# Kernel tuning notes

Measured on AMD Instinct MI355X. Metric: run time of the kernel, lower is better.

Reference implementation:

```python
import jax, jax.numpy as jnp
import numpy as np

C, H = 256, 256  # feat_num, feat_h (equirect is H x 2H)


def setup_inputs() -> dict:
    key = jax.random.key(0)
    ks = jax.random.split(key, 6)
    m = jax.random.normal(ks[0], (1, C, H, 2 * H), jnp.float32)
    b = jax.random.normal(ks[1], (1, C, H, H), jnp.float32)
    u = jax.random.normal(ks[2], (1, C, H, H), jnp.float32)
    d = jax.random.normal(ks[3], (1, C, H, H), jnp.float32)
    Wf = jax.random.normal(ks[4], (C, C, 3, 3), jnp.float32) * 0.02
    bf = jnp.zeros((C,), jnp.float32)
    Wm = jax.random.normal(ks[5], (1, 2 * C, 1, 1), jnp.float32) * 0.02
    bm = jnp.zeros((1,), jnp.float32)
    return {"m": m, "b": b, "u": u, "d": d, "Wf": Wf, "bf": bf, "Wm": Wm, "bm": bm}


def _cube2equi(cube, out_h, out_w):
    # cube: [6, C, h, h]; face order: 0 back(z-), 1 down(y-), 2 front(z+), 3 left(x-), 4 right(x+), 5 up(y+)
    h = cube.shape[-1]
    theta = (jnp.arange(out_w, dtype=cube.dtype) + 0.5) / out_w * (2.0 * jnp.pi) - jnp.pi  # longitude [-pi, pi)
    phi = jnp.pi / 2 - (jnp.arange(out_h, dtype=cube.dtype) + 0.5) / out_h * jnp.pi        # latitude [pi/2, -pi/2]
    st, ct = jnp.sin(theta)[None, :], jnp.cos(theta)[None, :]
    sp, cp = jnp.sin(phi)[:, None], jnp.cos(phi)[:, None]
    dx = cp * st
    dy = jnp.broadcast_to(sp, (out_h, out_w))
    dz = cp * ct
    ax, ay, az = jnp.abs(dx), jnp.abs(dy), jnp.abs(dz)
    mx = jnp.maximum(jnp.maximum(ax, ay), az)
    px, py, pz = dx / mx, dy / mx, dz / mx
    cond_z = (az >= ax) & (az >= ay)
    cond_x = (~cond_z) & (ax >= ay)
    face = jnp.where(cond_z, jnp.where(dz > 0, 2, 0),
           jnp.where(cond_x, jnp.where(dx > 0, 4, 3),
                              jnp.where(dy > 0, 5, 1)))
    a = jnp.where(cond_z, jnp.where(dz > 0, px, -px),
        jnp.where(cond_x, jnp.where(dx > 0, -pz, pz), px))
    bcoord = jnp.where(cond_z | cond_x, -py, jnp.where(dy > 0, pz, -pz))
    uu = jnp.clip((a + 1.0) * 0.5 * (h - 1), 0.0, h - 1)
    vv = jnp.clip((bcoord + 1.0) * 0.5 * (h - 1), 0.0, h - 1)
    u0 = jnp.floor(uu).astype(jnp.int32); v0 = jnp.floor(vv).astype(jnp.int32)
    u1 = jnp.minimum(u0 + 1, h - 1); v1 = jnp.minimum(v0 + 1, h - 1)
    wu = uu - u0; wv = vv - v0

    def samp(vi, ui):
        return cube[face, :, vi, ui]  # [out_h, out_w, C] gather over all channels

    out = (samp(v0, u0) * ((1 - wv) * (1 - wu))[..., None]
         + samp(v0, u1) * ((1 - wv) * wu)[..., None]
         + samp(v1, u0) * (wv * (1 - wu))[..., None]
         + samp(v1, u1) * (wv * wu)[..., None])
    return jnp.transpose(out, (2, 0, 1))  # [C, out_h, out_w]


def _conv(x, w, bias, pad):
    y = jax.lax.conv_general_dilated(x, w, (1, 1), [(pad, pad), (pad, pad)],
                                     dimension_numbers=("NCHW", "OIHW", "NCHW"))
    return y + bias[None, :, None, None]


def reference(m, b, u, d, Wf, bf, Wm, bm):
    h = b.shape[-1]
    empty = jnp.zeros_like(b[0])  # the torch module's zero 'emptyFace' parameter
    # faces stacked as [back, down, empty, empty, empty, up], vectorized over all channels
    cube = jnp.stack([b[0], d[0], empty, empty, empty, u[0]])  # [6, C, h, h]
    aux = _cube2equi(cube, h, 2 * h)[None]                      # [1, C, h, 2h]
    M_aux = jax.nn.relu(_conv(aux, Wf, bf, 1))
    M_main = jax.nn.relu(_conv(m, Wf, bf, 1))
    mask = jax.nn.sigmoid(_conv(jnp.concatenate([M_main, M_aux], axis=1), Wm, bm, 0))
    return m + mask * M_aux
```

## Files before the change

kernel.cpp:

```cpp
#include <hip/hip_runtime.h>
#include <hip/hip_bf16.h>

#define NPIX 131072
#define WP   514
#define XP_BYTES 67897344
#define XP_STRIDE 67962880

typedef __attribute__((ext_vector_type(8))) short bf16x8;
typedef __attribute__((ext_vector_type(4))) float f32x4;

typedef const __attribute__((address_space(1))) void g_cvoid;
typedef __attribute__((address_space(3))) void l_void;

__device__ __forceinline__ void async16(const void* g, void* l) {
  __builtin_amdgcn_global_load_lds((g_cvoid*)g, (l_void*)l, 16, 0, 0);
}

__global__ void zero_borders(__hip_bfloat16* Xm, __hip_bfloat16* Xa) {
  int i = blockIdx.x;
  __hip_bfloat16* X = blockIdx.y ? Xa : Xm;
  long ppix;
  if (i < 514)       ppix = i;
  else if (i < 1028) ppix = 257L * WP + (i - 514);
  else if (i < 1284) ppix = (long)(i - 1028 + 1) * WP;
  else               ppix = (long)(i - 1284 + 1) * WP + 513;
  ((unsigned int*)(X + ppix * 256))[threadIdx.x] = 0u;
}

__global__ void zero_mask(float* maskacc) {
  maskacc[blockIdx.x * 256 + threadIdx.x] = 0.f;
}

__global__ void prep_weights(const float* __restrict__ Wf, __hip_bfloat16* __restrict__ Wtt) {
  int idx = blockIdx.x * 256 + threadIdx.x;
  int cout = idx / 2304, rem = idx % 2304;
  int o = rem >> 8, ci = rem & 255;
  Wtt[(((o << 5) + (ci >> 3)) << 11) + (cout << 3) + (ci & 7)] =
      __float2bfloat16(Wf[(cout * 256 + ci) * 9 + o]);
}

__global__ void nchw_to_pad_nhwc(const float* __restrict__ src, __hip_bfloat16* __restrict__ Xp) {
  __shared__ __align__(16) __hip_bfloat16 tile[64 * 264];
  int tid = threadIdx.x;
  int p0 = blockIdx.x * 64;
  int px = tid & 63, w = tid >> 6;
  for (int k = 0; k < 64; ++k) {
    int c = (k << 2) + w;
    tile[px * 264 + c] = __float2bfloat16(src[(long)c * NPIX + p0 + px]);
  }
  __syncthreads();
  int y = p0 >> 9, x0 = p0 & 511;
  long basep = (long)(y + 1) * WP + x0 + 1;
  for (int pass = 0; pass < 8; ++pass) {
    int tpx = (pass << 3) + (tid >> 5);
    int chunk = tid & 31;
    uint4 v = *(const uint4*)&tile[tpx * 264 + (chunk << 3)];
    *(uint4*)&Xp[(basep + tpx) * 256 + (chunk << 3)] = v;
  }
}

__global__ void aux_gen(const float* __restrict__ fb, const float* __restrict__ fd,
                        const float* __restrict__ fu,
                        __hip_bfloat16* __restrict__ Xp) {
  __shared__ __align__(16) __hip_bfloat16 tile[64 * 264];
  int tid = threadIdx.x;
  int p0 = blockIdx.x * 64;
  int px = tid & 63, w = tid >> 6;

  int p = p0 + px;
  int yy = p >> 9, xx = p & 511;
  float theta = ((xx + 0.5f) / 512.f) * 6.283185307179586f - 3.141592653589793f;
  float phi   = 1.5707963267948966f - ((yy + 0.5f) / 256.f) * 3.141592653589793f;
  float st = sinf(theta), ct = cosf(theta);
  float sp = sinf(phi),   cp = cosf(phi);
  float dx = cp * st, dy = sp, dz = cp * ct;
  float ax = fabsf(dx), ay = fabsf(dy), az = fabsf(dz);
  float mx = fmaxf(fmaxf(ax, ay), az);
  float pxn = dx / mx, pyn = dy / mx, pzn = dz / mx;
  bool cz = (az >= ax) && (az >= ay);
  bool cx = (!cz) && (ax >= ay);
  int face; float a, b;
  if (cz)      { face = dz > 0.f ? 2 : 0; a = dz > 0.f ? pxn : -pxn; b = -pyn; }
  else if (cx) { face = dx > 0.f ? 4 : 3; a = dx > 0.f ? -pzn : pzn; b = -pyn; }
  else         { face = dy > 0.f ? 5 : 1; a = pxn; b = dy > 0.f ? pzn : -pzn; }
  float uu = fminf(fmaxf((a + 1.f) * 0.5f * 255.f, 0.f), 255.f);
  float vv = fminf(fmaxf((b + 1.f) * 0.5f * 255.f, 0.f), 255.f);

  const float* F = (face == 0) ? fb : (face == 1) ? fd : (face == 5) ? fu : nullptr;
  int u0 = (int)uu, v0 = (int)vv;
  int u1 = min(u0 + 1, 255), v1 = min(v0 + 1, 255);
  float wu = uu - (float)u0, wv = vv - (float)v0;
  float w00 = (1.f - wv) * (1.f - wu), w01 = (1.f - wv) * wu;
  float w10 = wv * (1.f - wu),         w11 = wv * wu;
  int i00 = v0 * 256 + u0, i01 = v0 * 256 + u1;
  int i10 = v1 * 256 + u0, i11 = v1 * 256 + u1;
  for (int k = 0; k < 64; ++k) {
    int c = (k << 2) + w;
    float val = 0.f;
    if (F) {
      const float* Fc = F + ((long)c << 16);
      val = w00 * Fc[i00] + w01 * Fc[i01] + w10 * Fc[i10] + w11 * Fc[i11];
    }
    tile[px * 264 + c] = __float2bfloat16(val);
  }
  __syncthreads();
  int y = p0 >> 9, x0g = p0 & 511;
  long basep = (long)(y + 1) * WP + x0g + 1;
  for (int pass = 0; pass < 8; ++pass) {
    int tpx = (pass << 3) + (tid >> 5);
    int chunk = tid & 31;
    uint4 v = *(const uint4*)&tile[tpx * 264 + (chunk << 3)];
    *(uint4*)&Xp[(basep + tpx) * 256 + (chunk << 3)] = v;
  }
}

template <bool STORE>
__global__ void conv3x3_mfma(const __hip_bfloat16* __restrict__ Xp,
                             const __hip_bfloat16* __restrict__ Wtt,
                             const float* __restrict__ bias,
                             const float* __restrict__ wm,
                             __hip_bfloat16* __restrict__ Out,
                             float* __restrict__ maskacc) {
  __shared__ __align__(16) __hip_bfloat16 At[4 * 80 * 32];
  const int tid = threadIdx.x;
  const int wave = tid >> 6, lane = tid & 63;
  const int bx = blockIdx.x;
  const int n0 = (bx & 1) << 7;
  const int tile = bx >> 1;
  const int x0 = (tile >> 7) << 6;
  const int y0 = (tile & 127) << 1;
  const int wrow = wave >> 1;
  const int n_off = (wave & 1) << 6;
  const int lq = lane >> 4, ln = lane & 15;

  const long stage_row = (long)(y0 + wave) * WP + x0;
  const int s_col = lane >> 2;
  const int s_ci  = (lane & 3) << 3;

  f32x4 acc[4][4] = {};

  for (int s = 0; s < 8; ++s) {
    const int ci0 = s << 5;
#pragma unroll
    for (int j = 0; j < 5; ++j) {
      const __hip_bfloat16* gp = Xp + ((stage_row + (j << 4) + s_col) << 8) + ci0 + s_ci;
      async16(gp, &At[(wave * 80 + (j << 4)) << 5]);
    }
    __syncthreads();
#pragma unroll
    for (int o = 0; o < 9; ++o) {
      const int dy = o / 3, dxo = o % 3;
      const int arow = (wrow + dy) * 80;
      bf16x8 af[4], bb[4];
#pragma unroll
      for (int mi = 0; mi < 4; ++mi)
        af[mi] = *(const bf16x8*)&At[((arow + mi * 16 + ln + dxo) << 5) + (lq << 3)];
#pragma unroll
      for (int ni = 0; ni < 4; ++ni)
        bb[ni] = *(const bf16x8*)&Wtt[(((o << 5) + (s << 2) + lq) << 11) +
                                      ((n0 + n_off + ni * 16 + ln) << 3)];
#pragma unroll
      for (int mi = 0; mi < 4; ++mi)
#pragma unroll
        for (int ni = 0; ni < 4; ++ni)
          acc[mi][ni] = __builtin_amdgcn_mfma_f32_16x16x32_bf16(af[mi], bb[ni], acc[mi][ni], 0, 0, 0);
    }
    __syncthreads();
  }

  float bv[4], wv[4];
#pragma unroll
  for (int ni = 0; ni < 4; ++ni) {
    int cc = n0 + n_off + ni * 16 + ln;
    bv[ni] = bias[cc];
    wv[ni] = wm[cc];
  }
  const int prow = (y0 + wrow) * 512 + x0;
#pragma unroll
  for (int mi = 0; mi < 4; ++mi) {
#pragma unroll
    for (int r = 0; r < 4; ++r) {
      int pix = prow + mi * 16 + (lq << 2) + r;
      float mp = 0.f;
#pragma unroll
      for (int ni = 0; ni < 4; ++ni) {
        float v = acc[mi][ni][r] + bv[ni];
        v = v > 0.f ? v : 0.f;
        if (STORE) Out[((long)pix << 8) + (n0 + n_off + ni * 16 + ln)] = __float2bfloat16(v);
        mp += v * wv[ni];
      }
      mp += __shfl_xor(mp, 1);
      mp += __shfl_xor(mp, 2);
      mp += __shfl_xor(mp, 4);
      mp += __shfl_xor(mp, 8);
      if (ln == 0) atomicAdd(&maskacc[pix], mp);
    }
  }
}

__global__ void mask_sigmoid(float* maskacc, const float* __restrict__ bm) {
  int i = blockIdx.x * 256 + threadIdx.x;
  float v = maskacc[i] + bm[0];
  maskacc[i] = 1.f / (1.f + expf(-v));
}

__global__ void final_combine(const float* __restrict__ m,
                              const __hip_bfloat16* __restrict__ MauxT,
                              const float* __restrict__ mask,
                              float* __restrict__ out) {
  __shared__ __align__(16) __hip_bfloat16 tile[64 * 264];
  __shared__ float sm[64];
  int tid = threadIdx.x;
  int p0 = blockIdx.x * 64;
  if (tid < 64) sm[tid] = mask[p0 + tid];
#pragma unroll
  for (int j = 0; j < 8; ++j) {
    int f = j * 256 + tid;
    int px = f >> 5, c8 = f & 31;
    *(uint4*)&tile[px * 264 + (c8 << 3)] =
        *(const uint4*)&MauxT[(((long)(p0 + px)) << 8) + (c8 << 3)];
  }
  __syncthreads();
  int px = tid & 63, w = tid >> 6;
  float mk = sm[px];
  for (int k = 0; k < 64; ++k) {
    int c = (k << 2) + w;
    long gi = (long)c * NPIX + p0 + px;
    out[gi] = m[gi] + mk * __bfloat162float(tile[px * 264 + c]);
  }
}

extern "C" void kernel_launch(void* const* d_in, const int* in_sizes, int n_in,
                              void* d_out, int out_size, void* d_ws, size_t ws_size,
                              hipStream_t stream) {
  const float* m  = (const float*)d_in[0];
  const float* fb = (const float*)d_in[1];
  const float* fu = (const float*)d_in[2];
  const float* fd = (const float*)d_in[3];
  const float* Wf = (const float*)d_in[4];
  const float* bf = (const float*)d_in[5];
  const float* Wm = (const float*)d_in[6];
  const float* bm = (const float*)d_in[7];
  float* out = (float*)d_out;

  char* ws = (char*)d_ws;
  __hip_bfloat16* Xp_m   = (__hip_bfloat16*)(ws);
  __hip_bfloat16* Xp_aux = (__hip_bfloat16*)(ws + (size_t)XP_STRIDE);
  __hip_bfloat16* Wtt    = (__hip_bfloat16*)(ws + 2uL * XP_STRIDE);
  __hip_bfloat16* MauxT  = (__hip_bfloat16*)(ws + 2uL * XP_STRIDE + 1179648);
  float* maskacc         = (float*)(ws + 2uL * XP_STRIDE + 1179648 + 67108864);

  zero_borders<<<dim3(1540, 2), 128, 0, stream>>>(Xp_m, Xp_aux);
  zero_mask<<<512, 256, 0, stream>>>(maskacc);
  prep_weights<<<2304, 256, 0, stream>>>(Wf, Wtt);
  nchw_to_pad_nhwc<<<2048, 256, 0, stream>>>(m, Xp_m);
  aux_gen<<<2048, 256, 0, stream>>>(fb, fd, fu, Xp_aux);
  conv3x3_mfma<true><<<2048, 256, 0, stream>>>(Xp_aux, Wtt, bf, Wm + 256, MauxT, maskacc);
  conv3x3_mfma<false><<<2048, 256, 0, stream>>>(Xp_m, Wtt, bf, Wm, nullptr, maskacc);
  mask_sigmoid<<<512, 256, 0, stream>>>(maskacc, bm);
  final_combine<<<2048, 256, 0, stream>>>(m, MauxT, maskacc, out);
}
```

Measured before the change: 832.7 us.

## Transpose cube faces to NHWC bf16 before gathering in cube-to-equirect sampling

Adds a pre-pass that converts the three used cube faces into an NHWC bf16 buffer, so the cube-to-equirect resampling can read each bilinear tap as contiguous 16-byte channel vectors. A new aux_gen_v2 maps one wavefront to each output pixel, with lane pairs splitting the horizontal taps and combining them by shuffle. Pixels on empty faces are written as zeros directly. This replaces the strided NCHW fp32 gathers with coalesced reads. The cost is an extra 96MB workspace and an extra transpose pass, and the buffer is aliased with Xp_m, so the order of launches matters. The original path is kept as a fallback when the workspace is too small.

```diff
diff --git a/kernel.cpp b/kernel.cpp
--- a/kernel.cpp
+++ b/kernel.cpp
@@ -5,6 +5,7 @@
 #define WP   514
 #define XP_BYTES 67897344
 #define XP_STRIDE 67962880
+#define FT_BYTES 100663296
 
 typedef __attribute__((ext_vector_type(8))) short bf16x8;
 typedef __attribute__((ext_vector_type(4))) float f32x4;
@@ -56,6 +57,90 @@
     int chunk = tid & 31;
     uint4 v = *(const uint4*)&tile[tpx * 264 + (chunk << 3)];
     *(uint4*)&Xp[(basep + tpx) * 256 + (chunk << 3)] = v;
+  }
+}
+
+__global__ void face_to_nhwc(const float* __restrict__ fb, const float* __restrict__ fd,
+                             const float* __restrict__ fu, __hip_bfloat16* __restrict__ Ft) {
+  __shared__ __align__(16) __hip_bfloat16 tile[64 * 264];
+  int tid = threadIdx.x;
+  int face = blockIdx.x >> 10;
+  int p0 = (blockIdx.x & 1023) << 6;
+  const float* src = (face == 0) ? fb : (face == 1) ? fd : fu;
+  int px = tid & 63, w = tid >> 6;
+  for (int k = 0; k < 64; ++k) {
+    int c = (k << 2) + w;
+    tile[px * 264 + c] = __float2bfloat16(src[(long)c * 65536 + p0 + px]);
+  }
+  __syncthreads();
+  long basep = ((long)face << 16) + p0;
+  for (int pass = 0; pass < 8; ++pass) {
+    int tpx = (pass << 3) + (tid >> 5);
+    int chunk = tid & 31;
+    uint4 v = *(const uint4*)&tile[tpx * 264 + (chunk << 3)];
+    *(uint4*)&Ft[((basep + tpx) << 8) + (chunk << 3)] = v;
+  }
+}
+
+__device__ __forceinline__ void bf8_fma(uint4 q, float w, float* acc) {
+  unsigned x;
+  x = q.x; acc[0] += w * __uint_as_float(x << 16); acc[1] += w * __uint_as_float(x & 0xffff0000u);
+  x = q.y; acc[2] += w * __uint_as_float(x << 16); acc[3] += w * __uint_as_float(x & 0xffff0000u);
+  x = q.z; acc[4] += w * __uint_as_float(x << 16); acc[5] += w * __uint_as_float(x & 0xffff0000u);
+  x = q.w; acc[6] += w * __uint_as_float(x << 16); acc[7] += w * __uint_as_float(x & 0xffff0000u);
+}
+
+__global__ void aux_gen_v2(const __hip_bfloat16* __restrict__ Ft,
+                           __hip_bfloat16* __restrict__ Xp) {
+  const int lane = threadIdx.x & 63;
+  const int p = (blockIdx.x << 2) + (threadIdx.x >> 6);
+  const int yy = p >> 9, xx = p & 511;
+
+  float theta = ((xx + 0.5f) / 512.f) * 6.283185307179586f - 3.141592653589793f;
+  float phi   = 1.5707963267948966f - ((yy + 0.5f) / 256.f) * 3.141592653589793f;
+  float st = sinf(theta), ct = cosf(theta);
+  float sp = sinf(phi),   cp = cosf(phi);
+  float dx = cp * st, dy = sp, dz = cp * ct;
+  float ax = fabsf(dx), ay = fabsf(dy), az = fabsf(dz);
+  float mx = fmaxf(fmaxf(ax, ay), az);
+  float pxn = dx / mx, pyn = dy / mx, pzn = dz / mx;
+  bool cz = (az >= ax) && (az >= ay);
+  bool cx = (!cz) && (ax >= ay);
+  int face; float a, b;
+  if (cz)      { face = dz > 0.f ? 2 : 0; a = dz > 0.f ? pxn : -pxn; b = -pyn; }
+  else if (cx) { face = dx > 0.f ? 4 : 3; a = dx > 0.f ? -pzn : pzn; b = -pyn; }
+  else         { face = dy > 0.f ? 5 : 1; a = pxn; b = dy > 0.f ? pzn : -pzn; }
+  float uu = fminf(fmaxf((a + 1.f) * 0.5f * 255.f, 0.f), 255.f);
+  float vv = fminf(fmaxf((b + 1.f) * 0.5f * 255.f, 0.f), 255.f);
+
+  const long outbase = ((long)((yy + 1) * WP + xx + 1)) << 8;
+  const int c0 = (lane >> 1) << 3;
+  const int up = lane & 1;
+  const int slot = (face == 0) ? 0 : (face == 1) ? 1 : (face == 5) ? 2 : -1;
+
+  if (slot < 0) {
+    if (!up) *(uint4*)&Xp[outbase + c0] = make_uint4(0u, 0u, 0u, 0u);
+    return;
+  }
+  int u0 = (int)uu, v0 = (int)vv;
+  int u1 = min(u0 + 1, 255), v1 = min(v0 + 1, 255);
+  float wu = uu - (float)u0, wv = vv - (float)v0;
+  int uc = up ? u1 : u0;
+  float wA = up ? wu : (1.f - wu);
+  const __hip_bfloat16* base = Ft + ((long)slot << 24);
+
+  float acc[8] = {0.f, 0.f, 0.f, 0.f, 0.f, 0.f, 0.f, 0.f};
+  uint4 q0 = *(const uint4*)&base[(((long)(v0 << 8) + uc) << 8) + c0];
+  uint4 q1 = *(const uint4*)&base[(((long)(v1 << 8) + uc) << 8) + c0];
+  bf8_fma(q0, (1.f - wv) * wA, acc);
+  bf8_fma(q1, wv * wA, acc);
+#pragma unroll
+  for (int j = 0; j < 8; ++j) acc[j] += __shfl_xor(acc[j], 1);
+  if (!up) {
+    union { uint4 q; __hip_bfloat16 h[8]; } o;
+#pragma unroll
+    for (int j = 0; j < 8; ++j) o.h[j] = __float2bfloat16(acc[j]);
+    *(uint4*)&Xp[outbase + c0] = o.q;
   }
 }
 
@@ -244,19 +329,41 @@
   float* out = (float*)d_out;
 
   char* ws = (char*)d_ws;
-  __hip_bfloat16* Xp_m   = (__hip_bfloat16*)(ws);
-  __hip_bfloat16* Xp_aux = (__hip_bfloat16*)(ws + (size_t)XP_STRIDE);
-  __hip_bfloat16* Wtt    = (__hip_bfloat16*)(ws + 2uL * XP_STRIDE);
-  __hip_bfloat16* MauxT  = (__hip_bfloat16*)(ws + 2uL * XP_STRIDE + 1179648);
-  float* maskacc         = (float*)(ws + 2uL * XP_STRIDE + 1179648 + 67108864);
-
-  zero_borders<<<dim3(1540, 2), 128, 0, stream>>>(Xp_m, Xp_aux);
-  zero_mask<<<512, 256, 0, stream>>>(maskacc);
-  prep_weights<<<2304, 256, 0, stream>>>(Wf, Wtt);
-  nchw_to_pad_nhwc<<<2048, 256, 0, stream>>>(m, Xp_m);
-  aux_gen<<<2048, 256, 0, stream>>>(fb, fd, fu, Xp_aux);
-  conv3x3_mfma<true><<<2048, 256, 0, stream>>>(Xp_aux, Wtt, bf, Wm + 256, MauxT, maskacc);
-  conv3x3_mfma<false><<<2048, 256, 0, stream>>>(Xp_m, Wtt, bf, Wm, nullptr, maskacc);
-  mask_sigmoid<<<512, 256, 0, stream>>>(maskacc, bm);
-  final_combine<<<2048, 256, 0, stream>>>(m, MauxT, maskacc, out);
-}
+  const size_t NEED_FAST = (size_t)FT_BYTES + XP_STRIDE + 1179648 + 67108864 + 524288;
+
+  if (ws_size >= NEED_FAST) {
+    __hip_bfloat16* Ft     = (__hip_bfloat16*)(ws);
+    __hip_bfloat16* Xp_m   = (__hip_bfloat16*)(ws);
+    __hip_bfloat16* Xp_aux = (__hip_bfloat16*)(ws + (size_t)FT_BYTES);
+    __hip_bfloat16* Wtt    = (__hip_bfloat16*)(ws + (size_t)FT_BYTES + XP_STRIDE);
+    __hip_bfloat16* MauxT  = (__hip_bfloat16*)(ws + (size_t)FT_BYTES + XP_STRIDE + 1179648);
+    float* maskacc         = (float*)(ws + (size_t)FT_BYTES + XP_STRIDE + 1179648 + 67108864);
+
+    face_to_nhwc<<<3072, 256, 0, stream>>>(fb, fd, fu, Ft);
+    aux_gen_v2<<<32768, 256, 0, stream>>>(Ft, Xp_aux);
+    nchw_to_pad_nhwc<<<2048, 256, 0, stream>>>(m, Xp_m);
+    zero_borders<<<dim3(1540, 2), 128, 0, stream>>>(Xp_m, Xp_aux);
+    prep_weights<<<2304, 256, 0, stream>>>(Wf, Wtt);
+    zero_mask<<<512, 256, 0, stream>>>(maskacc);
+    conv3x3_mfma<true><<<2048, 256, 0, stream>>>(Xp_aux, Wtt, bf, Wm + 256, MauxT, maskacc);
+    conv3x3_mfma<false><<<2048, 256, 0, stream>>>(Xp_m, Wtt, bf, Wm, nullptr, maskacc);
+    mask_sigmoid<<<512, 256, 0, stream>>>(maskacc, bm);
+    final_combine<<<2048, 256, 0, stream>>>(m, MauxT, maskacc, out);
+  } else {
+    __hip_bfloat16* Xp_m   = (__hip_bfloat16*)(ws);
+    __hip_bfloat16* Xp_aux = (__hip_bfloat16*)(ws + (size_t)XP_STRIDE);
+    __hip_bfloat16* Wtt    = (__hip_bfloat16*)(ws + 2uL * XP_STRIDE);
+    __hip_bfloat16* MauxT  = (__hip_bfloat16*)(ws + 2uL * XP_STRIDE + 1179648);
+    float* maskacc         = (float*)(ws + 2uL * XP_STRIDE + 1179648 + 67108864);
+
+    zero_borders<<<dim3(1540, 2), 128, 0, stream>>>(Xp_m, Xp_aux);
+    zero_mask<<<512, 256, 0, stream>>>(maskacc);
+    prep_weights<<<2304, 256, 0, stream>>>(Wf, Wtt);
+    nchw_to_pad_nhwc<<<2048, 256, 0, stream>>>(m, Xp_m);
+    aux_gen<<<2048, 256, 0, stream>>>(fb, fd, fu, Xp_aux);
+    conv3x3_mfma<true><<<2048, 256, 0, stream>>>(Xp_aux, Wtt, bf, Wm + 256, MauxT, maskacc);
+    conv3x3_mfma<false><<<2048, 256, 0, stream>>>(Xp_m, Wtt, bf, Wm, nullptr, maskacc);
+    mask_sigmoid<<<512, 256, 0, stream>>>(maskacc, bm);
+    final_combine<<<2048, 256, 0, stream>>>(m, MauxT, maskacc, out);
+  }
+}
```

Result: faster. 755.2 us (-9.3%).
